# Optimization experiments

Measured on AMD Instinct MI355X. Metric: run time of the kernel, lower is better.

Reference implementation:

```python
import jax, jax.numpy as jnp
import numpy as np

N = 50000   # nodes
E = 800000  # edges (avg degree 16)
IN = 384    # input gene features
H = 256     # hidden
EPS = 1e-12 # F.normalize eps


def setup_inputs() -> dict:
    key = jax.random.key(0)
    ks = jax.random.split(key, 10)
    x = jax.random.uniform(ks[0], (N, IN), dtype=jnp.float32) * 10.0  # count-like
    src = jax.random.randint(ks[1], (E,), 0, N, dtype=jnp.int32)
    dst = jax.random.randint(ks[2], (E,), 0, N, dtype=jnp.int32)
    def lin(k, din):
        return (jax.random.normal(k, (din, H), dtype=jnp.float32) / np.sqrt(din).astype(np.float32))
    return {
        'x': x, 'src': src, 'dst': dst,
        'W_self0': lin(ks[3], IN), 'W_neigh0': lin(ks[4], IN), 'b0': jnp.zeros((H,), jnp.float32),
        'W_self1': lin(ks[5], H), 'W_neigh1': lin(ks[6], H), 'b1': jnp.zeros((H,), jnp.float32),
        'W_self2': lin(ks[7], H), 'W_neigh2': lin(ks[8], H), 'b2': jnp.zeros((H,), jnp.float32),
    }


def _sage_mean(h, src, dst, Ws, Wn, b):
    # gather neighbor feats along edges, mean-aggregate into dst nodes
    msg = h[src]                                             # [E, d]
    agg = jax.ops.segment_sum(msg, dst, num_segments=N)      # [N, d]
    deg = jax.ops.segment_sum(jnp.ones((E,), h.dtype), dst, num_segments=N)
    h_neigh = agg / jnp.maximum(deg, 1.0)[:, None]           # isolated nodes -> 0
    return h @ Ws + h_neigh @ Wn + b


def _l2norm(h):
    n = jnp.sqrt(jnp.sum(h * h, axis=-1, keepdims=True))
    return h / jnp.maximum(n, EPS)


def reference(x, src, dst, W_self0, W_neigh0, b0, W_self1, W_neigh1, b1, W_self2, W_neigh2, b2):
    h = jnp.log1p(x)
    # layers 0..n-2: SAGEConv -> relu -> L2 normalize
    h = _l2norm(jax.nn.relu(_sage_mean(h, src, dst, W_self0, W_neigh0, b0)))
    h = _l2norm(jax.nn.relu(_sage_mean(h, src, dst, W_self1, W_neigh1, b1)))
    # last layer: plain SAGEConv (feat_drop inactive in eval)
    h = _sage_mean(h, src, dst, W_self2, W_neigh2, b2)
    return h
```

## Files before the change

### kernel.cpp

```cpp
#include <hip/hip_runtime.h>
#include <hip/hip_bf16.h>

#define N_NODES 50000
#define N_EDGES 800000
#define DIM_IN  384
#define DIM_H   256

typedef __bf16 bf16x8 __attribute__((ext_vector_type(8)));
typedef float  f32x4  __attribute__((ext_vector_type(4)));

static __device__ __forceinline__ ushort f2bf(float f) {
  uint u = __float_as_uint(f);
  u += 0x7fffu + ((u >> 16) & 1u);
  return (ushort)(u >> 16);
}
static __device__ __forceinline__ float bf_lo(uint u) { return __uint_as_float(u << 16); }
static __device__ __forceinline__ float bf_hi(uint u) { return __uint_as_float(u & 0xffff0000u); }

typedef const __attribute__((address_space(1))) void* gas_p;
typedef __attribute__((address_space(3))) void* las_p;
static __device__ __forceinline__ void gload16(const void* g, void* l) {
  __builtin_amdgcn_global_load_lds((gas_p)g, (las_p)l, 16, 0, 0);
}

static __device__ __forceinline__ float log1p_fast(float x) {
  return __logf(1.0f + x);
}

static __device__ __forceinline__ int permc(int p) {
  return ((p >> 7) << 7) + ((p & 7) << 4) + ((p >> 3) & 15);
}
static __device__ __forceinline__ void pack_one(const float* W, ushort* out, int local, bool perm) {
  int k = local >> 8, col = local & 255;
  int kc = k >> 5, kgd = (k >> 3) & 3, e = k & 7;
  int kgs = kgd ^ ((col >> 1) & 3);
  int krow = perm ? permc(k) : k;
  out[((size_t)kc * 256 + col) * 32 + kgs * 8 + e] = f2bf(W[krow * 256 + col]);
}

#define HIST_BLOCKS 3125
#define L1_BLOCKS   18750
#define STRIPE1_TOT (HIST_BLOCKS * 7)
#define PACK_TOT (2 * DIM_IN * 256 + 4 * DIM_H * 256)
#define PACK_BLOCKS ((PACK_TOT + 255) / 256)

__global__ void prep_kernel(const float* __restrict__ x, ushort* __restrict__ h,
                            const int* __restrict__ dst, int* __restrict__ deg,
                            const float* W0s, const float* W0n, const float* W1s,
                            const float* W1n, const float* W2s, const float* W2n,
                            ushort* o0s, ushort* o0n, ushort* o1s, ushort* o1n,
                            ushort* o2s, ushort* o2n) {
  int bid = blockIdx.x;
  if (bid < STRIPE1_TOT) {
    int g = bid / 7, r = bid - g * 7;
    if (r == 0) {
      int i = g * 256 + threadIdx.x;
      if (i < N_EDGES) atomicAdd(&deg[dst[i]], 1);
    } else {
      int i = (g * 6 + (r - 1)) * 256 + threadIdx.x;
      float4 v = reinterpret_cast<const float4*>(x)[i];
      ushort4 o;
      o.x = f2bf(log1p_fast(v.x));
      o.y = f2bf(log1p_fast(v.y));
      o.z = f2bf(log1p_fast(v.z));
      o.w = f2bf(log1p_fast(v.w));
      reinterpret_cast<ushort4*>(h)[i] = o;
    }
  } else {
    int idx = (bid - STRIPE1_TOT) * 256 + threadIdx.x;
    const int SZ0 = DIM_IN * 256;
    const int SZ1 = DIM_H * 256;
    if (idx < SZ0) pack_one(W0s, o0s, idx, false);
    else if (idx < 2 * SZ0) pack_one(W0n, o0n, idx - SZ0, false);
    else if (idx < PACK_TOT) {
      int j = idx - 2 * SZ0;
      int w = j / SZ1, local = j - w * SZ1;
      if (w == 0) pack_one(W1s, o1s, local, true);
      else if (w == 1) pack_one(W1n, o1n, local, true);
      else if (w == 2) pack_one(W2s, o2s, local, true);
      else pack_one(W2n, o2n, local, true);
    }
  }
}

__global__ void scan1_kernel(const int* __restrict__ deg, int* __restrict__ tmp,
                             int* __restrict__ bsum) {
  __shared__ int buf[256];
  int t = threadIdx.x, i = blockIdx.x * 256 + t;
  int v = (i < N_NODES) ? deg[i] : 0;
  buf[t] = v;
  __syncthreads();
  int x = v;
#pragma unroll
  for (int off = 1; off < 256; off <<= 1) {
    int y = (t >= off) ? buf[t - off] : 0;
    __syncthreads();
    x += y;
    buf[t] = x;
    __syncthreads();
  }
  if (i < N_NODES) tmp[i] = x - v;
  if (t == 255) bsum[blockIdx.x] = x;
}

__global__ void scan2_kernel(int* __restrict__ bsum, int nb) {
  __shared__ int buf[256];
  int t = threadIdx.x;
  int v = (t < nb) ? bsum[t] : 0;
  buf[t] = v;
  __syncthreads();
  int x = v;
#pragma unroll
  for (int off = 1; off < 256; off <<= 1) {
    int y = (t >= off) ? buf[t - off] : 0;
    __syncthreads();
    x += y;
    buf[t] = x;
    __syncthreads();
  }
  if (t < nb) bsum[t] = x - v;
}

__global__ void scan3_kernel(const int* __restrict__ tmp, const int* __restrict__ bsum,
                             int* __restrict__ rowptr, int* __restrict__ cursor) {
  int i = blockIdx.x * 256 + threadIdx.x;
  if (i >= N_NODES) return;
  int r = tmp[i] + bsum[i >> 8];
  rowptr[i] = r;
  cursor[i] = r;
}

template <int K>
static __device__ void gemm_dual_body(int blk, ushort* Al, ushort* Bl, float* red,
                                      const ushort* __restrict__ A,
                                      const ushort* __restrict__ Bs,
                                      const ushort* __restrict__ Bn,
                                      const float* __restrict__ bias,
                                      ushort* __restrict__ Sout,
                                      unsigned char* __restrict__ Yq,
                                      float* __restrict__ scales) {
  constexpr int KC = K / 32;
  constexpr int NT = 2 * KC;
  const int tid = threadIdx.x;
  const int wv = tid >> 6, lane = tid & 63, lj = lane & 15, lg = lane >> 4;
  const int wm = wv >> 1, wn = wv & 1;
  const int r0 = blk * 128;

  int grow[2], akgd[2];
#pragma unroll
  for (int j = 0; j < 2; ++j) {
    int d = tid + j * 256;
    int row = d >> 2, kgs = d & 3;
    akgd[j] = kgs ^ ((row >> 1) & 3);
    int r = r0 + row;
    grow[j] = r < N_NODES ? r : N_NODES - 1;
  }

  int aoff[4], boff[8];
#pragma unroll
  for (int mf = 0; mf < 4; ++mf) {
    int row = wm * 64 + mf * 16 + lj;
    aoff[mf] = row * 32 + (lg ^ ((row >> 1) & 3)) * 8;
  }
#pragma unroll
  for (int f = 0; f < 8; ++f) {
    int col = wn * 128 + f * 16 + lj;
    boff[f] = col * 32 + (lg ^ ((col >> 1) & 3)) * 8;
  }

  auto stage = [&](int t, int bb) {
    int p = t >= KC;
    int kc = t - p * KC;
    const ushort* Bp = p ? Bn : Bs;
#pragma unroll
    for (int j = 0; j < 2; ++j)
      gload16(A + (size_t)grow[j] * K + kc * 32 + akgd[j] * 8,
              (char*)(Al + bb * 4096) + j * 4096 + wv * 1024);
#pragma unroll
    for (int j = 0; j < 4; ++j)
      gload16(Bp + (size_t)kc * 8192 + (tid + j * 256) * 8,
              (char*)(Bl + bb * 8192) + j * 4096 + wv * 1024);
  };

  float bvv[8];
#pragma unroll
  for (int f = 0; f < 8; ++f) bvv[f] = bias[wn * 128 + f * 16 + lj];

  f32x4 acc[4][8];
#pragma unroll
  for (int mf = 0; mf < 4; ++mf)
#pragma unroll
    for (int f = 0; f < 8; ++f) acc[mf][f] = (f32x4){0.f, 0.f, 0.f, 0.f};

  stage(0, 0);
  __syncthreads();
  int b = 0;
  for (int t = 0; t < NT; ++t) {
    if (t + 1 < NT) stage(t + 1, b ^ 1);
    bf16x8 av[4], bv[8];
#pragma unroll
    for (int mf = 0; mf < 4; ++mf)
      av[mf] = *reinterpret_cast<const bf16x8*>(Al + b * 4096 + aoff[mf]);
#pragma unroll
    for (int f = 0; f < 8; ++f)
      bv[f] = *reinterpret_cast<const bf16x8*>(Bl + b * 8192 + boff[f]);
#pragma unroll
    for (int mf = 0; mf < 4; ++mf)
#pragma unroll
      for (int f = 0; f < 8; ++f)
        acc[mf][f] = __builtin_amdgcn_mfma_f32_16x16x32_bf16(av[mf], bv[f], acc[mf][f], 0, 0, 0);
    if (t == KC - 1) {
#pragma unroll
      for (int mf = 0; mf < 4; ++mf)
#pragma unroll
        for (int e = 0; e < 4; ++e) {
          int row = r0 + wm * 64 + mf * 16 + lg * 4 + e;
          if (row < N_NODES) {
            ushort* pS = Sout + (size_t)row * 256 + wn * 128 + lj * 8;
            uint4 o;
            o.x = (uint)f2bf(acc[mf][0][e] + bvv[0]) | ((uint)f2bf(acc[mf][1][e] + bvv[1]) << 16);
            o.y = (uint)f2bf(acc[mf][2][e] + bvv[2]) | ((uint)f2bf(acc[mf][3][e] + bvv[3]) << 16);
            o.z = (uint)f2bf(acc[mf][4][e] + bvv[4]) | ((uint)f2bf(acc[mf][5][e] + bvv[5]) << 16);
            o.w = (uint)f2bf(acc[mf][6][e] + bvv[6]) | ((uint)f2bf(acc[mf][7][e] + bvv[7]) << 16);
            *reinterpret_cast<uint4*>(pS) = o;
          }
        }
#pragma unroll
      for (int mf = 0; mf < 4; ++mf)
#pragma unroll
        for (int f = 0; f < 8; ++f) acc[mf][f] = (f32x4){0.f, 0.f, 0.f, 0.f};
    }
    __syncthreads();
    b ^= 1;
  }

  float rmax[4][4];
#pragma unroll
  for (int mf = 0; mf < 4; ++mf)
#pragma unroll
    for (int e = 0; e < 4; ++e) {
      float m = 0.f;
#pragma unroll
      for (int f = 0; f < 8; ++f) m = fmaxf(m, fabsf(acc[mf][f][e]));
      m = fmaxf(m, __shfl_xor(m, 1));
      m = fmaxf(m, __shfl_xor(m, 2));
      m = fmaxf(m, __shfl_xor(m, 4));
      m = fmaxf(m, __shfl_xor(m, 8));
      rmax[mf][e] = m;
    }
  if (lj == 0) {
#pragma unroll
    for (int mf = 0; mf < 4; ++mf)
#pragma unroll
      for (int e = 0; e < 4; ++e)
        red[(wn * 2 + wm) * 64 + mf * 16 + lg * 4 + e] = rmax[mf][e];
  }
  __syncthreads();
#pragma unroll
  for (int mf = 0; mf < 4; ++mf)
#pragma unroll
    for (int e = 0; e < 4; ++e) {
      float m = fmaxf(fmaxf(red[(0 * 2 + wm) * 64 + mf * 16 + lg * 4 + e],
                            red[(1 * 2 + wm) * 64 + mf * 16 + lg * 4 + e]), 1e-30f);
      float inv_s = 127.0f / m;
      int row = r0 + wm * 64 + mf * 16 + lg * 4 + e;
      if (row < N_NODES) {
        uint lo = 0, hi = 0;
#pragma unroll
        for (int f = 0; f < 4; ++f) {
          int q = (int)rintf(acc[mf][f][e] * inv_s) + 128;
          q = max(0, min(255, q));
          lo |= (uint)q << (8 * f);
        }
#pragma unroll
        for (int f = 4; f < 8; ++f) {
          int q = (int)rintf(acc[mf][f][e] * inv_s) + 128;
          q = max(0, min(255, q));
          hi |= (uint)q << (8 * (f - 4));
        }
        *reinterpret_cast<uint2*>(Yq + (size_t)row * 256 + wn * 128 + lj * 8) = make_uint2(lo, hi);
        if (wn == 0 && lj == 0) scales[row] = m * (1.0f / 127.0f);
      }
    }
}

#define GEMM_BLOCKS ((N_NODES + 127) / 128)
#define GF_TOT (GEMM_BLOCKS * 9)

__global__ __launch_bounds__(256, 2) void gemm0_fill_kernel(
    const ushort* __restrict__ A, const ushort* __restrict__ Bs,
    const ushort* __restrict__ Bn, const float* __restrict__ bias,
    ushort* __restrict__ Sout, unsigned char* __restrict__ Yq, float* __restrict__ scales,
    const int* __restrict__ src, const int* __restrict__ dst,
    int* __restrict__ cursor, ushort* __restrict__ csr) {
  __shared__ ushort Al[2 * 4096];
  __shared__ ushort Bl[2 * 8192];
  __shared__ float red[256];
  int g = blockIdx.x / 9, r = blockIdx.x - g * 9;
  if (r == 0) {
    gemm_dual_body<DIM_IN>(g, Al, Bl, red, A, Bs, Bn, bias, Sout, Yq, scales);
  } else {
    int i = (g * 8 + (r - 1)) * 256 + threadIdx.x;
    if (i < N_EDGES) {
      int d = dst[i];
      int p = atomicAdd(&cursor[d], 1);
      csr[p] = (ushort)src[i];
    }
  }
}

__global__ __launch_bounds__(256, 2) void gemm_dual_kernel(
    const ushort* __restrict__ A, const ushort* __restrict__ Bs,
    const ushort* __restrict__ Bn, const float* __restrict__ bias,
    ushort* __restrict__ Sout, unsigned char* __restrict__ Yq, float* __restrict__ scales) {
  __shared__ ushort Al[2 * 4096];
  __shared__ ushort Bl[2 * 8192];
  __shared__ float red[256];
  gemm_dual_body<DIM_H>(blockIdx.x, Al, Bl, red, A, Bs, Bn, bias, Sout, Yq, scales);
}

template <bool FINAL>
__global__ __launch_bounds__(256) void gather_kernel(const unsigned char* __restrict__ Yq,
                                                     const float* __restrict__ scales,
                                                     const ushort* __restrict__ Sin,
                                                     const int* __restrict__ rowptr,
                                                     const int* __restrict__ deg,
                                                     const ushort* __restrict__ csr,
                                                     void* __restrict__ outv) {
  int node = blockIdx.x * 8 + (threadIdx.x >> 5);
  if (node >= N_NODES) return;
  int hl = threadIdx.x & 31;
  int start = rowptr[node];
  int d = deg[node];
  float acc[8];
#pragma unroll
  for (int i = 0; i < 8; ++i) acc[i] = 0.0f;
  float stot = 0.f;

  auto ub = [](uint u, int j) { return (float)((u >> (8 * j)) & 0xffu); };
  int e = 0;
  for (; e + 4 <= d; e += 4) {
    int s0 = csr[start + e], s1 = csr[start + e + 1];
    int s2 = csr[start + e + 2], s3 = csr[start + e + 3];
    float c0 = scales[s0], c1 = scales[s1], c2 = scales[s2], c3 = scales[s3];
    uint2 q0 = *reinterpret_cast<const uint2*>(Yq + (size_t)s0 * 256 + hl * 8);
    uint2 q1 = *reinterpret_cast<const uint2*>(Yq + (size_t)s1 * 256 + hl * 8);
    uint2 q2 = *reinterpret_cast<const uint2*>(Yq + (size_t)s2 * 256 + hl * 8);
    uint2 q3 = *reinterpret_cast<const uint2*>(Yq + (size_t)s3 * 256 + hl * 8);
    stot += c0 + c1 + c2 + c3;
#pragma unroll
    for (int j = 0; j < 4; ++j) {
      acc[j]     += c0 * ub(q0.x, j) + c1 * ub(q1.x, j) + c2 * ub(q2.x, j) + c3 * ub(q3.x, j);
      acc[4 + j] += c0 * ub(q0.y, j) + c1 * ub(q1.y, j) + c2 * ub(q2.y, j) + c3 * ub(q3.y, j);
    }
  }
  for (; e < d; ++e) {
    int s = csr[start + e];
    float c = scales[s];
    uint2 q = *reinterpret_cast<const uint2*>(Yq + (size_t)s * 256 + hl * 8);
    stot += c;
#pragma unroll
    for (int j = 0; j < 4; ++j) {
      acc[j]     += c * ub(q.x, j);
      acc[4 + j] += c * ub(q.y, j);
    }
  }

  float invd = 1.0f / fmaxf((float)d, 1.0f);
  float nb[8];
#pragma unroll
  for (int j = 0; j < 8; ++j) nb[j] = (acc[j] - 128.0f * stot) * invd;

  uint4 sv = *reinterpret_cast<const uint4*>(Sin + (size_t)node * 256 + hl * 8);
  uint su[4] = {sv.x, sv.y, sv.z, sv.w};

  if constexpr (FINAL) {
    float* out = (float*)outv + (size_t)node * 256 + (hl >> 4) * 128 + (hl & 15);
#pragma unroll
    for (int i = 0; i < 4; ++i) {
      out[(2 * i) * 16]     = nb[2 * i] + bf_lo(su[i]);
      out[(2 * i + 1) * 16] = nb[2 * i + 1] + bf_hi(su[i]);
    }
  } else {
    float v[8];
    float ssq = 0.f;
#pragma unroll
    for (int i = 0; i < 4; ++i) {
      float a = fmaxf(nb[2 * i] + bf_lo(su[i]), 0.0f);
      float b = fmaxf(nb[2 * i + 1] + bf_hi(su[i]), 0.0f);
      v[2 * i] = a; v[2 * i + 1] = b;
      ssq += a * a + b * b;
    }
    ssq += __shfl_xor(ssq, 1);
    ssq += __shfl_xor(ssq, 2);
    ssq += __shfl_xor(ssq, 4);
    ssq += __shfl_xor(ssq, 8);
    ssq += __shfl_xor(ssq, 16);
    float rn = 1.0f / fmaxf(sqrtf(ssq), 1e-12f);
    uint o[4];
#pragma unroll
    for (int i = 0; i < 4; ++i) {
      uint lo = f2bf(v[2 * i] * rn);
      uint hi = f2bf(v[2 * i + 1] * rn);
      o[i] = lo | (hi << 16);
    }
    *reinterpret_cast<uint4*>((ushort*)outv + (size_t)node * 256 + hl * 8) =
        make_uint4(o[0], o[1], o[2], o[3]);
  }
}

extern "C" void kernel_launch(void* const* d_in, const int* in_sizes, int n_in,
                              void* d_out, int out_size, void* d_ws, size_t ws_size,
                              hipStream_t stream) {
  const float* x   = (const float*)d_in[0];
  const int*   src = (const int*)d_in[1];
  const int*   dst = (const int*)d_in[2];
  const float* Ws0 = (const float*)d_in[3];
  const float* Wn0 = (const float*)d_in[4];
  const float* b0  = (const float*)d_in[5];
  const float* Ws1 = (const float*)d_in[6];
  const float* Wn1 = (const float*)d_in[7];
  const float* b1  = (const float*)d_in[8];
  const float* Ws2 = (const float*)d_in[9];
  const float* Wn2 = (const float*)d_in[10];
  const float* b2  = (const float*)d_in[11];

  uintptr_t p = ((uintptr_t)d_ws + 255) & ~(uintptr_t)255;
  auto carve = [&](size_t bytes) {
    void* r = (void*)p;
    p += (bytes + 255) & ~(size_t)255;
    return r;
  };
  ushort* h0 = (ushort*)carve((size_t)N_NODES * DIM_IN * 2);
  ushort* h2 = h0;
  ushort* S_mid = (ushort*)carve((size_t)N_NODES * DIM_H * 2);
  ushort* h1 = (ushort*)carve((size_t)N_NODES * DIM_H * 2);
  unsigned char* Yq = (unsigned char*)carve((size_t)N_NODES * 256);
  float* scales = (float*)carve((size_t)N_NODES * 4);
  ushort* Ws0p = (ushort*)carve((size_t)DIM_IN * 256 * 2);
  ushort* Wn0p = (ushort*)carve((size_t)DIM_IN * 256 * 2);
  ushort* Ws1p = (ushort*)carve((size_t)DIM_H * 256 * 2);
  ushort* Wn1p = (ushort*)carve((size_t)DIM_H * 256 * 2);
  ushort* Ws2p = (ushort*)carve((size_t)DIM_H * 256 * 2);
  ushort* Wn2p = (ushort*)carve((size_t)DIM_H * 256 * 2);
  int* deg    = (int*)carve((size_t)N_NODES * 4);
  int* rowptr = (int*)carve((size_t)N_NODES * 4);
  int* cursor = (int*)carve((size_t)N_NODES * 4);
  int* stmp   = (int*)carve((size_t)N_NODES * 4);
  int* bsum   = (int*)carve(256 * 4);
  ushort* csr = (ushort*)carve((size_t)N_EDGES * 2);

  hipMemsetAsync(deg, 0, (size_t)N_NODES * 4, stream);

  prep_kernel<<<STRIPE1_TOT + PACK_BLOCKS, 256, 0, stream>>>(
      x, h0, dst, deg, Ws0, Wn0, Ws1, Wn1, Ws2, Wn2,
      Ws0p, Wn0p, Ws1p, Wn1p, Ws2p, Wn2p);

  const int scanBlocks = (N_NODES + 255) / 256;
  scan1_kernel<<<scanBlocks, 256, 0, stream>>>(deg, stmp, bsum);
  scan2_kernel<<<1, 256, 0, stream>>>(bsum, scanBlocks);
  scan3_kernel<<<scanBlocks, 256, 0, stream>>>(stmp, bsum, rowptr, cursor);

  gemm0_fill_kernel<<<GF_TOT, 256, 0, stream>>>(h0, Ws0p, Wn0p, b0, S_mid, Yq, scales,
                                                src, dst, cursor, csr);

  const int gatherBlocks = (N_NODES + 7) / 8;

  gather_kernel<false><<<gatherBlocks, 256, 0, stream>>>(Yq, scales, S_mid, rowptr, deg, csr, h1);
  gemm_dual_kernel<<<GEMM_BLOCKS, 256, 0, stream>>>(h1, Ws1p, Wn1p, b1, S_mid, Yq, scales);
  gather_kernel<false><<<gatherBlocks, 256, 0, stream>>>(Yq, scales, S_mid, rowptr, deg, csr, h2);
  gemm_dual_kernel<<<GEMM_BLOCKS, 256, 0, stream>>>(h2, Ws2p, Wn2p, b2, S_mid, Yq, scales);
  gather_kernel<true><<<gatherBlocks, 256, 0, stream>>>(Yq, scales, S_mid, rowptr, deg, csr, d_out);
}
```

Baseline: 298.0 us.

## Record edge rank during degree count to fill CSR without second atomic pass

The degree-count atomicAdd now stores each edge's returned rank, so the CSR fill computes its slot as rowptr[dst]+rank with no atomics and no cursor array. Fill blocks are moved after all GEMM blocks instead of being interleaved, and each thread handles four edges. Launch bounds for the GEMM kernels go from 2 to 3 waves per SIMD, which may force register spills. The change adds an extra rank array write and read (2 bytes per edge).

```diff
diff --git a/kernel.cpp b/kernel.cpp
--- a/kernel.cpp
+++ b/kernel.cpp
@@ -46,6 +46,7 @@
 
 __global__ void prep_kernel(const float* __restrict__ x, ushort* __restrict__ h,
                             const int* __restrict__ dst, int* __restrict__ deg,
+                            ushort* __restrict__ rank,
                             const float* W0s, const float* W0n, const float* W1s,
                             const float* W1n, const float* W2s, const float* W2n,
                             ushort* o0s, ushort* o0n, ushort* o1s, ushort* o1n,
@@ -55,7 +56,10 @@
     int g = bid / 7, r = bid - g * 7;
     if (r == 0) {
       int i = g * 256 + threadIdx.x;
-      if (i < N_EDGES) atomicAdd(&deg[dst[i]], 1);
+      if (i < N_EDGES) {
+        int rr = atomicAdd(&deg[dst[i]], 1);
+        rank[i] = (ushort)rr;
+      }
     } else {
       int i = (g * 6 + (r - 1)) * 256 + threadIdx.x;
       float4 v = reinterpret_cast<const float4*>(x)[i];
@@ -122,12 +126,10 @@
 }
 
 __global__ void scan3_kernel(const int* __restrict__ tmp, const int* __restrict__ bsum,
-                             int* __restrict__ rowptr, int* __restrict__ cursor) {
+                             int* __restrict__ rowptr) {
   int i = blockIdx.x * 256 + threadIdx.x;
   if (i >= N_NODES) return;
-  int r = tmp[i] + bsum[i >> 8];
-  rowptr[i] = r;
-  cursor[i] = r;
+  rowptr[i] = tmp[i] + bsum[i >> 8];
 }
 
 template <int K>
@@ -285,31 +287,32 @@
 }
 
 #define GEMM_BLOCKS ((N_NODES + 127) / 128)
-#define GF_TOT (GEMM_BLOCKS * 9)
-
-__global__ __launch_bounds__(256, 2) void gemm0_fill_kernel(
+#define FILL_BLOCKS ((N_EDGES + 1023) / 1024)
+
+__global__ __launch_bounds__(256, 3) void gemm0_fill_kernel(
     const ushort* __restrict__ A, const ushort* __restrict__ Bs,
     const ushort* __restrict__ Bn, const float* __restrict__ bias,
     ushort* __restrict__ Sout, unsigned char* __restrict__ Yq, float* __restrict__ scales,
     const int* __restrict__ src, const int* __restrict__ dst,
-    int* __restrict__ cursor, ushort* __restrict__ csr) {
+    const int* __restrict__ rowptr, const ushort* __restrict__ rank,
+    ushort* __restrict__ csr) {
   __shared__ ushort Al[2 * 4096];
   __shared__ ushort Bl[2 * 8192];
   __shared__ float red[256];
-  int g = blockIdx.x / 9, r = blockIdx.x - g * 9;
-  if (r == 0) {
-    gemm_dual_body<DIM_IN>(g, Al, Bl, red, A, Bs, Bn, bias, Sout, Yq, scales);
+  if (blockIdx.x < GEMM_BLOCKS) {
+    gemm_dual_body<DIM_IN>(blockIdx.x, Al, Bl, red, A, Bs, Bn, bias, Sout, Yq, scales);
   } else {
-    int i = (g * 8 + (r - 1)) * 256 + threadIdx.x;
-    if (i < N_EDGES) {
-      int d = dst[i];
-      int p = atomicAdd(&cursor[d], 1);
-      csr[p] = (ushort)src[i];
-    }
-  }
-}
-
-__global__ __launch_bounds__(256, 2) void gemm_dual_kernel(
+    int base = (blockIdx.x - GEMM_BLOCKS) * 1024 + threadIdx.x * 4;
+#pragma unroll
+    for (int j = 0; j < 4; ++j) {
+      int i = base + j;
+      if (i < N_EDGES)
+        csr[rowptr[dst[i]] + rank[i]] = (ushort)src[i];
+    }
+  }
+}
+
+__global__ __launch_bounds__(256, 3) void gemm_dual_kernel(
     const ushort* __restrict__ A, const ushort* __restrict__ Bs,
     const ushort* __restrict__ Bn, const float* __restrict__ bias,
     ushort* __restrict__ Sout, unsigned char* __restrict__ Yq, float* __restrict__ scales) {
@@ -445,24 +448,24 @@
   ushort* Wn2p = (ushort*)carve((size_t)DIM_H * 256 * 2);
   int* deg    = (int*)carve((size_t)N_NODES * 4);
   int* rowptr = (int*)carve((size_t)N_NODES * 4);
-  int* cursor = (int*)carve((size_t)N_NODES * 4);
   int* stmp   = (int*)carve((size_t)N_NODES * 4);
   int* bsum   = (int*)carve(256 * 4);
-  ushort* csr = (ushort*)carve((size_t)N_EDGES * 2);
+  ushort* rank = (ushort*)carve((size_t)N_EDGES * 2);
+  ushort* csr  = (ushort*)carve((size_t)N_EDGES * 2);
 
   hipMemsetAsync(deg, 0, (size_t)N_NODES * 4, stream);
 
   prep_kernel<<<STRIPE1_TOT + PACK_BLOCKS, 256, 0, stream>>>(
-      x, h0, dst, deg, Ws0, Wn0, Ws1, Wn1, Ws2, Wn2,
+      x, h0, dst, deg, rank, Ws0, Wn0, Ws1, Wn1, Ws2, Wn2,
       Ws0p, Wn0p, Ws1p, Wn1p, Ws2p, Wn2p);
 
   const int scanBlocks = (N_NODES + 255) / 256;
   scan1_kernel<<<scanBlocks, 256, 0, stream>>>(deg, stmp, bsum);
   scan2_kernel<<<1, 256, 0, stream>>>(bsum, scanBlocks);
-  scan3_kernel<<<scanBlocks, 256, 0, stream>>>(stmp, bsum, rowptr, cursor);
-
-  gemm0_fill_kernel<<<GF_TOT, 256, 0, stream>>>(h0, Ws0p, Wn0p, b0, S_mid, Yq, scales,
-                                                src, dst, cursor, csr);
+  scan3_kernel<<<scanBlocks, 256, 0, stream>>>(stmp, bsum, rowptr);
+
+  gemm0_fill_kernel<<<GEMM_BLOCKS + FILL_BLOCKS, 256, 0, stream>>>(
+      h0, Ws0p, Wn0p, b0, S_mid, Yq, scales, src, dst, rowptr, rank, csr);
 
   const int gatherBlocks = (N_NODES + 7) / 8;
 
```

Result: slower. 383.4 us (+28.7%).

## Fuse neighbor gather/normalize with next-layer dual GEMM into one kernel

Applied to the files above, without the earlier changes.

Merges the gather+relu+L2norm step of layers 0 and 1 with the following layer's self/neighbor GEMM into one kernel. The normalized 64-row tile stays in LDS as the A operand, so the bf16 hidden activations are never written to or re-read from global memory. Yq and scale buffers are ping-ponged so one kernel does not overwrite the input it is still reading. The cost is a smaller 64-row GEMM tile, a different weight permutation for layer 2 and a final gather with scattered output columns, plus less parallelism during the gather phase.

```diff
diff --git a/kernel.cpp b/kernel.cpp
--- a/kernel.cpp
+++ b/kernel.cpp
@@ -27,19 +27,21 @@
   return __logf(1.0f + x);
 }
 
-static __device__ __forceinline__ int permc(int p) {
+static __device__ __forceinline__ int permc128(int p) {
   return ((p >> 7) << 7) + ((p & 7) << 4) + ((p >> 3) & 15);
 }
-static __device__ __forceinline__ void pack_one(const float* W, ushort* out, int local, bool perm) {
+static __device__ __forceinline__ int permc64(int p) {
+  return ((p >> 6) << 6) + ((p & 3) << 4) + ((p >> 2) & 15);
+}
+static __device__ __forceinline__ void pack_one(const float* W, ushort* out, int local, int mode) {
   int k = local >> 8, col = local & 255;
   int kc = k >> 5, kgd = (k >> 3) & 3, e = k & 7;
   int kgs = kgd ^ ((col >> 1) & 3);
-  int krow = perm ? permc(k) : k;
+  int krow = (mode == 1) ? permc128(k) : (mode == 2) ? permc64(k) : k;
   out[((size_t)kc * 256 + col) * 32 + kgs * 8 + e] = f2bf(W[krow * 256 + col]);
 }
 
 #define HIST_BLOCKS 3125
-#define L1_BLOCKS   18750
 #define STRIPE1_TOT (HIST_BLOCKS * 7)
 #define PACK_TOT (2 * DIM_IN * 256 + 4 * DIM_H * 256)
 #define PACK_BLOCKS ((PACK_TOT + 255) / 256)
@@ -70,15 +72,15 @@
     int idx = (bid - STRIPE1_TOT) * 256 + threadIdx.x;
     const int SZ0 = DIM_IN * 256;
     const int SZ1 = DIM_H * 256;
-    if (idx < SZ0) pack_one(W0s, o0s, idx, false);
-    else if (idx < 2 * SZ0) pack_one(W0n, o0n, idx - SZ0, false);
+    if (idx < SZ0) pack_one(W0s, o0s, idx, 0);
+    else if (idx < 2 * SZ0) pack_one(W0n, o0n, idx - SZ0, 0);
     else if (idx < PACK_TOT) {
       int j = idx - 2 * SZ0;
       int w = j / SZ1, local = j - w * SZ1;
-      if (w == 0) pack_one(W1s, o1s, local, true);
-      else if (w == 1) pack_one(W1n, o1n, local, true);
-      else if (w == 2) pack_one(W2s, o2s, local, true);
-      else pack_one(W2n, o2n, local, true);
+      if (w == 0) pack_one(W1s, o1s, local, 1);
+      else if (w == 1) pack_one(W1n, o1n, local, 1);
+      else if (w == 2) pack_one(W2s, o2s, local, 2);
+      else pack_one(W2n, o2n, local, 2);
     }
   }
 }
@@ -284,8 +286,8 @@
     }
 }
 
-#define GEMM_BLOCKS ((N_NODES + 127) / 128)
-#define GF_TOT (GEMM_BLOCKS * 9)
+#define GEMM0_BLOCKS ((N_NODES + 127) / 128)
+#define GF_TOT (GEMM0_BLOCKS * 9)
 
 __global__ __launch_bounds__(256, 2) void gemm0_fill_kernel(
     const ushort* __restrict__ A, const ushort* __restrict__ Bs,
@@ -309,24 +311,215 @@
   }
 }
 
-__global__ __launch_bounds__(256, 2) void gemm_dual_kernel(
-    const ushort* __restrict__ A, const ushort* __restrict__ Bs,
-    const ushort* __restrict__ Bn, const float* __restrict__ bias,
-    ushort* __restrict__ Sout, unsigned char* __restrict__ Yq, float* __restrict__ scales) {
-  __shared__ ushort Al[2 * 4096];
-  __shared__ ushort Bl[2 * 8192];
+#define FUSED_BLOCKS ((N_NODES + 63) / 64)
+
+__global__ __launch_bounds__(256, 2) void fused_gg_kernel(
+    const unsigned char* __restrict__ Yq_in, const float* __restrict__ sc_in,
+    const int* __restrict__ rowptr, const int* __restrict__ deg,
+    const ushort* __restrict__ csr,
+    const ushort* __restrict__ Bs, const ushort* __restrict__ Bn,
+    const float* __restrict__ bias,
+    ushort* __restrict__ S_io,
+    unsigned char* __restrict__ Yq_out, float* __restrict__ sc_out) {
+  __shared__ ushort Aful[8 * 2048];
+  __shared__ ushort Bl[2][8192];
   __shared__ float red[256];
-  gemm_dual_body<DIM_H>(blockIdx.x, Al, Bl, red, A, Bs, Bn, bias, Sout, Yq, scales);
-}
-
-template <bool FINAL>
-__global__ __launch_bounds__(256) void gather_kernel(const unsigned char* __restrict__ Yq,
-                                                     const float* __restrict__ scales,
-                                                     const ushort* __restrict__ Sin,
-                                                     const int* __restrict__ rowptr,
-                                                     const int* __restrict__ deg,
-                                                     const ushort* __restrict__ csr,
-                                                     void* __restrict__ outv) {
+
+  const int tid = threadIdx.x;
+  const int wv = tid >> 6, lane = tid & 63, lj = lane & 15, lg = lane >> 4;
+  const int hw = tid >> 5, hl = tid & 31;
+  const int r0 = blockIdx.x * 64;
+
+  auto stageB = [&](int t, int bb) {
+    int ph = t >> 3;
+    int kc = t & 7;
+    const ushort* Bp = ph ? Bn : Bs;
+#pragma unroll
+    for (int j = 0; j < 4; ++j)
+      gload16(Bp + (size_t)kc * 8192 + (tid + j * 256) * 8,
+              (char*)&Bl[bb][0] + j * 4096 + wv * 1024);
+  };
+
+  stageB(0, 0);
+
+  auto ub = [](uint u, int j) { return (float)((u >> (8 * j)) & 0xffu); };
+  for (int it = 0; it < 8; ++it) {
+    int row = it * 8 + hw;
+    int node = r0 + row;
+    if (node < N_NODES) {
+      int start = rowptr[node];
+      int d = deg[node];
+      float acc[8];
+#pragma unroll
+      for (int i = 0; i < 8; ++i) acc[i] = 0.f;
+      float stot = 0.f;
+      int e = 0;
+      for (; e + 4 <= d; e += 4) {
+        int s0 = csr[start + e], s1 = csr[start + e + 1];
+        int s2 = csr[start + e + 2], s3 = csr[start + e + 3];
+        float c0 = sc_in[s0], c1 = sc_in[s1], c2 = sc_in[s2], c3 = sc_in[s3];
+        uint2 q0 = *reinterpret_cast<const uint2*>(Yq_in + (size_t)s0 * 256 + hl * 8);
+        uint2 q1 = *reinterpret_cast<const uint2*>(Yq_in + (size_t)s1 * 256 + hl * 8);
+        uint2 q2 = *reinterpret_cast<const uint2*>(Yq_in + (size_t)s2 * 256 + hl * 8);
+        uint2 q3 = *reinterpret_cast<const uint2*>(Yq_in + (size_t)s3 * 256 + hl * 8);
+        stot += c0 + c1 + c2 + c3;
+#pragma unroll
+        for (int j = 0; j < 4; ++j) {
+          acc[j]     += c0 * ub(q0.x, j) + c1 * ub(q1.x, j) + c2 * ub(q2.x, j) + c3 * ub(q3.x, j);
+          acc[4 + j] += c0 * ub(q0.y, j) + c1 * ub(q1.y, j) + c2 * ub(q2.y, j) + c3 * ub(q3.y, j);
+        }
+      }
+      for (; e < d; ++e) {
+        int s = csr[start + e];
+        float c = sc_in[s];
+        uint2 q = *reinterpret_cast<const uint2*>(Yq_in + (size_t)s * 256 + hl * 8);
+        stot += c;
+#pragma unroll
+        for (int j = 0; j < 4; ++j) {
+          acc[j]     += c * ub(q.x, j);
+          acc[4 + j] += c * ub(q.y, j);
+        }
+      }
+      float invd = 1.0f / fmaxf((float)d, 1.0f);
+      float nb[8];
+#pragma unroll
+      for (int j = 0; j < 8; ++j) nb[j] = (acc[j] - 128.0f * stot) * invd;
+
+      uint4 sv = *reinterpret_cast<const uint4*>(S_io + (size_t)node * 256 + hl * 8);
+      uint su[4] = {sv.x, sv.y, sv.z, sv.w};
+      float v[8];
+      float ssq = 0.f;
+#pragma unroll
+      for (int i = 0; i < 4; ++i) {
+        float a = fmaxf(nb[2 * i] + bf_lo(su[i]), 0.0f);
+        float b = fmaxf(nb[2 * i + 1] + bf_hi(su[i]), 0.0f);
+        v[2 * i] = a; v[2 * i + 1] = b;
+        ssq += a * a + b * b;
+      }
+      ssq += __shfl_xor(ssq, 1);
+      ssq += __shfl_xor(ssq, 2);
+      ssq += __shfl_xor(ssq, 4);
+      ssq += __shfl_xor(ssq, 8);
+      ssq += __shfl_xor(ssq, 16);
+      float rn = 1.0f / fmaxf(sqrtf(ssq), 1e-12f);
+      uint o[4];
+#pragma unroll
+      for (int i = 0; i < 4; ++i) {
+        uint lo = f2bf(v[2 * i] * rn);
+        uint hi = f2bf(v[2 * i + 1] * rn);
+        o[i] = lo | (hi << 16);
+      }
+      int kc = hl >> 2;
+      int kgs = ((hl & 3) ^ ((row >> 1) & 3) ^ kc) & 3;
+      *reinterpret_cast<uint4*>(&Aful[(kc << 11) + row * 32 + kgs * 8]) =
+          make_uint4(o[0], o[1], o[2], o[3]);
+    }
+  }
+  __syncthreads();
+
+  int arow[4], aswz[4];
+#pragma unroll
+  for (int mf = 0; mf < 4; ++mf) {
+    int row = mf * 16 + lj;
+    arow[mf] = row * 32;
+    aswz[mf] = lg ^ ((row >> 1) & 3);
+  }
+  int boff[4];
+#pragma unroll
+  for (int f = 0; f < 4; ++f) {
+    int col = wv * 64 + f * 16 + lj;
+    boff[f] = col * 32 + (lg ^ ((col >> 1) & 3)) * 8;
+  }
+  float bvv[4];
+#pragma unroll
+  for (int f = 0; f < 4; ++f) bvv[f] = bias[wv * 64 + f * 16 + lj];
+
+  f32x4 acc2[4][4];
+#pragma unroll
+  for (int mf = 0; mf < 4; ++mf)
+#pragma unroll
+    for (int f = 0; f < 4; ++f) acc2[mf][f] = (f32x4){0.f, 0.f, 0.f, 0.f};
+
+  int b = 0;
+  for (int t = 0; t < 16; ++t) {
+    if (t + 1 < 16) stageB(t + 1, b ^ 1);
+    int kc = t & 7;
+    bf16x8 av[4], bv[4];
+#pragma unroll
+    for (int mf = 0; mf < 4; ++mf)
+      av[mf] = *reinterpret_cast<const bf16x8*>(
+          &Aful[(kc << 11) + arow[mf] + (((aswz[mf] ^ kc) & 3) << 3)]);
+#pragma unroll
+    for (int f = 0; f < 4; ++f)
+      bv[f] = *reinterpret_cast<const bf16x8*>(&Bl[b][boff[f]]);
+#pragma unroll
+    for (int mf = 0; mf < 4; ++mf)
+#pragma unroll
+      for (int f = 0; f < 4; ++f)
+        acc2[mf][f] = __builtin_amdgcn_mfma_f32_16x16x32_bf16(av[mf], bv[f], acc2[mf][f], 0, 0, 0);
+    if (t == 7) {
+#pragma unroll
+      for (int mf = 0; mf < 4; ++mf)
+#pragma unroll
+        for (int e = 0; e < 4; ++e) {
+          int row = r0 + mf * 16 + lg * 4 + e;
+          if (row < N_NODES) {
+            uint2 o;
+            o.x = (uint)f2bf(acc2[mf][0][e] + bvv[0]) | ((uint)f2bf(acc2[mf][1][e] + bvv[1]) << 16);
+            o.y = (uint)f2bf(acc2[mf][2][e] + bvv[2]) | ((uint)f2bf(acc2[mf][3][e] + bvv[3]) << 16);
+            *reinterpret_cast<uint2*>(S_io + (size_t)row * 256 + wv * 64 + lj * 4) = o;
+          }
+        }
+#pragma unroll
+      for (int mf = 0; mf < 4; ++mf)
+#pragma unroll
+        for (int f = 0; f < 4; ++f) acc2[mf][f] = (f32x4){0.f, 0.f, 0.f, 0.f};
+    }
+    __syncthreads();
+    b ^= 1;
+  }
+
+#pragma unroll
+  for (int mf = 0; mf < 4; ++mf)
+#pragma unroll
+    for (int e = 0; e < 4; ++e) {
+      float m = fmaxf(fmaxf(fabsf(acc2[mf][0][e]), fabsf(acc2[mf][1][e])),
+                      fmaxf(fabsf(acc2[mf][2][e]), fabsf(acc2[mf][3][e])));
+      m = fmaxf(m, __shfl_xor(m, 1));
+      m = fmaxf(m, __shfl_xor(m, 2));
+      m = fmaxf(m, __shfl_xor(m, 4));
+      m = fmaxf(m, __shfl_xor(m, 8));
+      if (lj == 0) red[wv * 64 + mf * 16 + lg * 4 + e] = m;
+    }
+  __syncthreads();
+#pragma unroll
+  for (int mf = 0; mf < 4; ++mf)
+#pragma unroll
+    for (int e = 0; e < 4; ++e) {
+      int lr = mf * 16 + lg * 4 + e;
+      float m = fmaxf(fmaxf(red[lr], red[64 + lr]), fmaxf(red[128 + lr], red[192 + lr]));
+      m = fmaxf(m, 1e-30f);
+      float inv_s = 127.0f / m;
+      int row = r0 + lr;
+      if (row < N_NODES) {
+        uint w = 0;
+#pragma unroll
+        for (int f = 0; f < 4; ++f) {
+          int q = (int)rintf(acc2[mf][f][e] * inv_s) + 128;
+          q = max(0, min(255, q));
+          w |= (uint)q << (8 * f);
+        }
+        *reinterpret_cast<uint*>(Yq_out + (size_t)row * 256 + wv * 64 + lj * 4) = w;
+        if (wv == 0 && lj == 0) sc_out[row] = m * (1.0f / 127.0f);
+      }
+    }
+}
+
+__global__ __launch_bounds__(256) void gather_final_kernel(
+    const unsigned char* __restrict__ Yq, const float* __restrict__ scales,
+    const ushort* __restrict__ Sin, const int* __restrict__ rowptr,
+    const int* __restrict__ deg, const ushort* __restrict__ csr,
+    float* __restrict__ out) {
   int node = blockIdx.x * 8 + (threadIdx.x >> 5);
   if (node >= N_NODES) return;
   int hl = threadIdx.x & 31;
@@ -367,45 +560,19 @@
   }
 
   float invd = 1.0f / fmaxf((float)d, 1.0f);
-  float nb[8];
-#pragma unroll
-  for (int j = 0; j < 8; ++j) nb[j] = (acc[j] - 128.0f * stot) * invd;
-
   uint4 sv = *reinterpret_cast<const uint4*>(Sin + (size_t)node * 256 + hl * 8);
   uint su[4] = {sv.x, sv.y, sv.z, sv.w};
-
-  if constexpr (FINAL) {
-    float* out = (float*)outv + (size_t)node * 256 + (hl >> 4) * 128 + (hl & 15);
-#pragma unroll
-    for (int i = 0; i < 4; ++i) {
-      out[(2 * i) * 16]     = nb[2 * i] + bf_lo(su[i]);
-      out[(2 * i + 1) * 16] = nb[2 * i + 1] + bf_hi(su[i]);
-    }
-  } else {
-    float v[8];
-    float ssq = 0.f;
-#pragma unroll
-    for (int i = 0; i < 4; ++i) {
-      float a = fmaxf(nb[2 * i] + bf_lo(su[i]), 0.0f);
-      float b = fmaxf(nb[2 * i + 1] + bf_hi(su[i]), 0.0f);
-      v[2 * i] = a; v[2 * i + 1] = b;
-      ssq += a * a + b * b;
-    }
-    ssq += __shfl_xor(ssq, 1);
-    ssq += __shfl_xor(ssq, 2);
-    ssq += __shfl_xor(ssq, 4);
-    ssq += __shfl_xor(ssq, 8);
-    ssq += __shfl_xor(ssq, 16);
-    float rn = 1.0f / fmaxf(sqrtf(ssq), 1e-12f);
-    uint o[4];
-#pragma unroll
-    for (int i = 0; i < 4; ++i) {
-      uint lo = f2bf(v[2 * i] * rn);
-      uint hi = f2bf(v[2 * i + 1] * rn);
-      o[i] = lo | (hi << 16);
-    }
-    *reinterpret_cast<uint4*>((ushort*)outv + (size_t)node * 256 + hl * 8) =
-        make_uint4(o[0], o[1], o[2], o[3]);
+  float* op = out + (size_t)node * 256;
+#pragma unroll
+  for (int i = 0; i < 4; ++i) {
+    float v0 = (acc[2 * i] - 128.0f * stot) * invd + bf_lo(su[i]);
+    float v1 = (acc[2 * i + 1] - 128.0f * stot) * invd + bf_hi(su[i]);
+    int p0 = hl * 8 + 2 * i;
+    int p1 = p0 + 1;
+    int c0 = ((p0 >> 6) << 6) | ((p0 & 3) << 4) | ((p0 >> 2) & 15);
+    int c1 = ((p1 >> 6) << 6) | ((p1 & 3) << 4) | ((p1 >> 2) & 15);
+    op[c0] = v0;
+    op[c1] = v1;
   }
 }
 
@@ -432,11 +599,11 @@
     return r;
   };
   ushort* h0 = (ushort*)carve((size_t)N_NODES * DIM_IN * 2);
-  ushort* h2 = h0;
   ushort* S_mid = (ushort*)carve((size_t)N_NODES * DIM_H * 2);
-  ushort* h1 = (ushort*)carve((size_t)N_NODES * DIM_H * 2);
-  unsigned char* Yq = (unsigned char*)carve((size_t)N_NODES * 256);
-  float* scales = (float*)carve((size_t)N_NODES * 4);
+  unsigned char* Yq_a = (unsigned char*)carve((size_t)N_NODES * 256);
+  unsigned char* Yq_b = (unsigned char*)carve((size_t)N_NODES * 256);
+  float* sc_a = (float*)carve((size_t)N_NODES * 4);
+  float* sc_b = (float*)carve((size_t)N_NODES * 4);
   ushort* Ws0p = (ushort*)carve((size_t)DIM_IN * 256 * 2);
   ushort* Wn0p = (ushort*)carve((size_t)DIM_IN * 256 * 2);
   ushort* Ws1p = (ushort*)carve((size_t)DIM_H * 256 * 2);
@@ -461,14 +628,14 @@
   scan2_kernel<<<1, 256, 0, stream>>>(bsum, scanBlocks);
   scan3_kernel<<<scanBlocks, 256, 0, stream>>>(stmp, bsum, rowptr, cursor);
 
-  gemm0_fill_kernel<<<GF_TOT, 256, 0, stream>>>(h0, Ws0p, Wn0p, b0, S_mid, Yq, scales,
-                                                src, dst, cursor, csr);
-
-  const int gatherBlocks = (N_NODES + 7) / 8;
-
-  gather_kernel<false><<<gatherBlocks, 256, 0, stream>>>(Yq, scales, S_mid, rowptr, deg, csr, h1);
-  gemm_dual_kernel<<<GEMM_BLOCKS, 256, 0, stream>>>(h1, Ws1p, Wn1p, b1, S_mid, Yq, scales);
-  gather_kernel<false><<<gatherBlocks, 256, 0, stream>>>(Yq, scales, S_mid, rowptr, deg, csr, h2);
-  gemm_dual_kernel<<<GEMM_BLOCKS, 256, 0, stream>>>(h2, Ws2p, Wn2p, b2, S_mid, Yq, scales);
-  gather_kernel<true><<<gatherBlocks, 256, 0, stream>>>(Yq, scales, S_mid, rowptr, deg, csr, d_out);
-}
+  gemm0_fill_kernel<<<GF_TOT, 256, 0, stream>>>(
+      h0, Ws0p, Wn0p, b0, S_mid, Yq_a, sc_a, src, dst, cursor, csr);
+
+  fused_gg_kernel<<<FUSED_BLOCKS, 256, 0, stream>>>(
+      Yq_a, sc_a, rowptr, deg, csr, Ws1p, Wn1p, b1, S_mid, Yq_b, sc_b);
+  fused_gg_kernel<<<FUSED_BLOCKS, 256, 0, stream>>>(
+      Yq_b, sc_b, rowptr, deg, csr, Ws2p, Wn2p, b2, S_mid, Yq_a, sc_a);
+
+  gather_final_kernel<<<(N_NODES + 7) / 8, 256, 0, stream>>>(
+      Yq_a, sc_a, S_mid, rowptr, deg, csr, (float*)d_out);
+}
```

After: 404.7 us. 35.8% more time.
